# Kernel tuning notes

Measured on AMD Instinct MI355X. Metric: run time of the kernel, lower is better.

Reference implementation:

```python
import jax, jax.numpy as jnp
import numpy as np

B, T, C, L, NH = 2, 512, 512, 3, 8
SD, AD, MT = 65, 17, 4096  # state_dim+1, act_dim+1, max_timestep
H4 = 4 * C
S = 3 * T
D = C // NH


def setup_inputs() -> dict:
    key = jax.random.key(0)
    keys = iter(jax.random.split(key, 64))

    def p(*shape):
        return jax.random.normal(next(keys), shape, dtype=jnp.float32) * 0.02

    inp = {
        "timesteps": jax.random.randint(next(keys), (B, T), 0, MT),
        "states": jax.random.randint(next(keys), (B, T), 0, SD),
        "actions": jax.random.randint(next(keys), (B, T), 0, AD),
        "returns_to_go": jax.random.normal(next(keys), (B, T, 1), dtype=jnp.float32),
        # embeddings / input projections
        "Wt": p(MT, C), "Ws": p(SD, C), "Wa": p(AD, C),
        "Wr_w": p(C, 1), "Wr_b": p(C),
        "ln_e_g": jnp.ones((C,), jnp.float32), "ln_e_b": jnp.zeros((C,), jnp.float32),
        # per-block params, stacked on leading L axis (torch Linear: y = x @ W.T + b)
        "Wq": p(L, C, C), "bq": p(L, C), "Wk": p(L, C, C), "bk": p(L, C),
        "Wv": p(L, C, C), "bv": p(L, C), "Wo": p(L, C, C), "bo": p(L, C),
        "W1": p(L, H4, C), "b1": p(L, H4), "W2": p(L, C, H4), "b2": p(L, C),
        "ln1_g": jnp.ones((L, C), jnp.float32), "ln1_b": jnp.zeros((L, C), jnp.float32),
        "ln2_g": jnp.ones((L, C), jnp.float32), "ln2_b": jnp.zeros((L, C), jnp.float32),
        # prediction heads
        "pr_w": p(1, C), "pr_b": p(1),
        "ps_w": p(SD, C), "ps_b": p(SD),
        "pa_w": p(AD, C), "pa_b": p(AD),
    }
    return inp


def _ln(x, g, b):
    m = jnp.mean(x, axis=-1, keepdims=True)
    v = jnp.mean((x - m) ** 2, axis=-1, keepdims=True)
    return (x - m) / jnp.sqrt(v + 1e-5) * g + b


def _block_causal_mask(s):
    # blocks of 3 (attend within rtg/state/action triple) OR lower-triangular
    i = jnp.arange(s)
    return ((i[:, None] // 3) == (i[None, :] // 3)) | (i[:, None] >= i[None, :])


def reference(timesteps, states, actions, returns_to_go,
              Wt, Ws, Wa, Wr_w, Wr_b, ln_e_g, ln_e_b,
              Wq, bq, Wk, bk, Wv, bv, Wo, bo,
              W1, b1, W2, b2, ln1_g, ln1_b, ln2_g, ln2_b,
              pr_w, pr_b, ps_w, ps_b, pa_w, pa_b):
    te = Wt[timesteps]                                  # [B,T,C]
    se = Ws[states] + te
    ae = Wa[actions] + te
    re = returns_to_go @ Wr_w.T + Wr_b + te
    # interleave (rtg, state, action) per timestep -> [B, 3T, C]
    h = jnp.stack((re, se, ae), axis=2).reshape(B, S, C)
    h = _ln(h, ln_e_g, ln_e_b)

    mask = _block_causal_mask(S)                        # [S,S] bool
    scale = 1.0 / np.sqrt(D)
    all_w, all_m = [], []
    for l in range(L):
        q = (h @ Wq[l].T + bq[l]).reshape(B, S, NH, D).transpose(0, 2, 1, 3)
        k = (h @ Wk[l].T + bk[l]).reshape(B, S, NH, D).transpose(0, 2, 1, 3)
        v = (h @ Wv[l].T + bv[l]).reshape(B, S, NH, D).transpose(0, 2, 1, 3)
        scores = jnp.einsum('bnsd,bntd->bnst', q, k) * scale
        scores = jnp.where(mask, scores, -jnp.inf)
        w = jax.nn.softmax(scores, axis=-1)             # [B,NH,S,S]
        att = jnp.einsum('bnst,bntd->bnsd', w, v).transpose(0, 2, 1, 3).reshape(B, S, C)
        h = h + (att @ Wo[l].T + bo[l])
        h = _ln(h, ln1_g[l], ln1_b[l])
        m = jax.nn.gelu(h @ W1[l].T + b1[l], approximate=False)  # [B,S,4C]
        h = h + (m @ W2[l].T + b2[l])
        h = _ln(h, ln2_g[l], ln2_b[l])
        all_w.append(w)
        all_m.append(m)

    # faithful to original: reshape splits seq into 3 contiguous chunks of T
    hr = h.reshape(B, 3, T, C)
    rtg_preds = hr[:, 2] @ pr_w.T + pr_b                # [B,T,1]
    state_preds = hr[:, 2] @ ps_w.T + ps_b              # [B,T,SD]
    action_preds = hr[:, 1] @ pa_w.T + pa_b             # [B,T,AD] (discrete -> no tanh)
    return (state_preds, action_preds, rtg_preds, jnp.stack(all_w), jnp.stack(all_m))
```

## Files before the change

kernel.cpp:

```cpp
#include <hip/hip_runtime.h>
#include <hip/hip_bf16.h>
#include <math.h>

#define B_ 2
#define T_ 512
#define C_ 512
#define L_ 3
#define NH_ 8
#define SD_ 65
#define AD_ 17
#define H4_ 2048
#define S_ 1536
#define D_ 64

typedef __hip_bfloat16 bf16;
typedef __bf16 bf16x8 __attribute__((ext_vector_type(8)));
typedef __bf16 bf16x4 __attribute__((ext_vector_type(4)));
typedef float f32x4 __attribute__((ext_vector_type(4)));

#define OFF_STATE  0
#define OFF_ACTION 66560
#define OFF_RTG    83968
#define OFF_W      84992
#define OFF_M      113331200ULL
#define OUT_TOTAL  132205568ULL

#define WS_HF     0ULL
#define WS_HB     6291456ULL
#define WS_QK     9437184ULL
#define WS_VT     15728640ULL
#define WS_WB     18874368ULL
#define WS_BIAS   25165824ULL
#define WS_MB     25171968ULL
#define WOFF_O    (3 * C_ * C_)
#define WOFF_1    (4 * C_ * C_)
#define WOFF_2    (4 * C_ * C_ + H4_ * C_)
#define WCONV_N   (4 * C_ * C_ + 2 * H4_ * C_)

__device__ __forceinline__ __bf16 tobf(float v) {
    union { __hip_bfloat16 h; __bf16 b; } u;
    u.h = __float2bfloat16(v);
    return u.b;
}

__device__ __forceinline__ void gload_lds16(const bf16* g, bf16* l) {
    __builtin_amdgcn_global_load_lds(
        (const __attribute__((address_space(1))) void*)g,
        (__attribute__((address_space(3))) void*)l,
        16, 0, 0);
}

#define MFMA_(a, b, c) __builtin_amdgcn_mfma_f32_16x16x32_bf16(a, b, c, 0, 0, 0)

__device__ __forceinline__ void block_reduce2(float& s1, float& s2, float* lds) {
    for (int off = 32; off >= 1; off >>= 1) {
        s1 += __shfl_xor(s1, off, 64);
        s2 += __shfl_xor(s2, off, 64);
    }
    int wave = threadIdx.x >> 6;
    if ((threadIdx.x & 63) == 0) { lds[wave] = s1; lds[wave + 4] = s2; }
    __syncthreads();
    s1 = lds[0] + lds[1] + lds[2] + lds[3];
    s2 = lds[4] + lds[5] + lds[6] + lds[7];
}

__global__ __launch_bounds__(256) void convw_kernel(
    const float* __restrict__ Wq, const float* __restrict__ Wk,
    const float* __restrict__ Wv, const float* __restrict__ Wo,
    const float* __restrict__ W1, const float* __restrict__ W2,
    const float* __restrict__ bq, const float* __restrict__ bk, const float* __restrict__ bv,
    bf16* __restrict__ dst, float* __restrict__ pbias)
{
    int i = (blockIdx.x * 256 + threadIdx.x) * 4;
    const float* src; int off;
    if      (i <     C_ * C_)            { src = Wq; off = i; }
    else if (i < 2 * C_ * C_)            { src = Wk; off = i -     C_ * C_; }
    else if (i < 3 * C_ * C_)            { src = Wv; off = i - 2 * C_ * C_; }
    else if (i < 4 * C_ * C_)            { src = Wo; off = i - 3 * C_ * C_; }
    else if (i < 4 * C_ * C_ + H4_ * C_) { src = W1; off = i - 4 * C_ * C_; }
    else                                 { src = W2; off = i - 4 * C_ * C_ - H4_ * C_; }
    f32x4 v = *(const f32x4*)(src + off);
    bf16x4 o;
#pragma unroll
    for (int j = 0; j < 4; j++) o[j] = tobf(v[j]);
    *(bf16x4*)(dst + i) = o;
    if (blockIdx.x == 0) {
        for (int j = threadIdx.x; j < 3 * C_; j += 256)
            pbias[j] = (j < C_) ? bq[j] : (j < 2 * C_) ? bk[j - C_] : bv[j - 2 * C_];
    }
}

__global__ __launch_bounds__(256) void embed_kernel(
    const int* __restrict__ timesteps, const int* __restrict__ states,
    const int* __restrict__ actions, const float* __restrict__ rtg,
    const float* __restrict__ Wt, const float* __restrict__ Ws, const float* __restrict__ Wa,
    const float* __restrict__ Wr_w, const float* __restrict__ Wr_b,
    const float* __restrict__ g, const float* __restrict__ bta,
    float* __restrict__ h, bf16* __restrict__ hb)
{
    int bid = blockIdx.x;
    int b = bid / S_, s = bid % S_;
    int t = s / 3, kind = s % 3;
    int tid = threadIdx.x;
    int bt = b * T_ + t;
    float vals[2];
    float s1 = 0.f, s2 = 0.f;
    int ts = timesteps[bt];
    for (int i = 0; i < 2; i++) {
        int c = tid + i * 256;
        float te = Wt[(size_t)ts * C_ + c];
        float v;
        if (kind == 0)
            v = rtg[bt] * Wr_w[c] + Wr_b[c] + te;
        else if (kind == 1)
            v = Ws[(size_t)states[bt] * C_ + c] + te;
        else
            v = Wa[(size_t)actions[bt] * C_ + c] + te;
        vals[i] = v; s1 += v; s2 += v * v;
    }
    __shared__ float lds[8];
    block_reduce2(s1, s2, lds);
    float mean = s1 / C_;
    float rstd = rsqrtf(s2 / C_ - mean * mean + 1e-5f);
    size_t rowoff = (size_t)bid * C_;
    for (int i = 0; i < 2; i++) {
        int c = tid + i * 256;
        float o = (vals[i] - mean) * rstd * g[c] + bta[c];
        h[rowoff + c] = o;
        hb[rowoff + c] = __float2bfloat16(o);
    }
}

__global__ __launch_bounds__(256) void ln_kernel(
    float* __restrict__ h, const float* __restrict__ g, const float* __restrict__ bta,
    bf16* __restrict__ hb)
{
    int bid = blockIdx.x;
    int tid = threadIdx.x;
    size_t rowoff = (size_t)bid * C_;
    float vals[2]; float s1 = 0.f, s2 = 0.f;
    for (int i = 0; i < 2; i++) {
        float v = h[rowoff + tid + i * 256];
        vals[i] = v; s1 += v; s2 += v * v;
    }
    __shared__ float lds[8];
    block_reduce2(s1, s2, lds);
    float mean = s1 / C_;
    float rstd = rsqrtf(s2 / C_ - mean * mean + 1e-5f);
    for (int i = 0; i < 2; i++) {
        int c = tid + i * 256;
        float o = (vals[i] - mean) * rstd * g[c] + bta[c];
        h[rowoff + c] = o;
        hb[rowoff + c] = __float2bfloat16(o);
    }
}

__global__ __launch_bounds__(256) void gemm_st_kernel(
    const bf16* __restrict__ A, const bf16* __restrict__ W,
    const float* __restrict__ bias, int M, int N, int K, int epi,
    bf16* __restrict__ out_bf, bf16* __restrict__ vT,
    float* __restrict__ out_f32, bf16* __restrict__ out_bfs)
{
    __shared__ bf16 lA[2][128 * 64];
    __shared__ bf16 lB[2][64 * 64];
    int tid = threadIdx.x;
    int wave = tid >> 6, lane = tid & 63;
    int quad = lane >> 4, l16 = lane & 15;
    int m0 = blockIdx.y * 128;
    int n0 = blockIdx.x * 64;
    int lrow = lane >> 3;
    int lcol = (lane & 7) * 8;
    const bf16* Ag = A + (size_t)m0 * K;
    const bf16* Wg = W + (size_t)n0 * K;
    f32x4 acc[4][2] = {};
    int NT = K / 64;

#pragma unroll
    for (int jj = 0; jj < 4; jj++) {
        int q = wave * 4 + jj;
        gload_lds16(Ag + (size_t)(q * 8 + lrow) * K + lcol, &lA[0][q * 512]);
    }
#pragma unroll
    for (int jj = 0; jj < 2; jj++) {
        int q = wave * 2 + jj;
        gload_lds16(Wg + (size_t)(q * 8 + lrow) * K + lcol, &lB[0][q * 512]);
    }
    __syncthreads();

    int rw = wave >> 1, cw = wave & 1;
    for (int t = 0; t < NT; t++) {
        int cur = t & 1, nxt = cur ^ 1;
        if (t + 1 < NT) {
            int k0 = (t + 1) * 64;
#pragma unroll
            for (int jj = 0; jj < 4; jj++) {
                int q = wave * 4 + jj;
                gload_lds16(Ag + (size_t)(q * 8 + lrow) * K + k0 + lcol, &lA[nxt][q * 512]);
            }
#pragma unroll
            for (int jj = 0; jj < 2; jj++) {
                int q = wave * 2 + jj;
                gload_lds16(Wg + (size_t)(q * 8 + lrow) * K + k0 + lcol, &lB[nxt][q * 512]);
            }
        }
#pragma unroll
        for (int ks = 0; ks < 2; ks++) {
            bf16x8 bfr0 = *(const bf16x8*)(&lB[cur][(cw * 32 + l16) * 64 + ks * 32 + quad * 8]);
            bf16x8 bfr1 = *(const bf16x8*)(&lB[cur][(cw * 32 + 16 + l16) * 64 + ks * 32 + quad * 8]);
#pragma unroll
            for (int mf = 0; mf < 4; mf++) {
                bf16x8 afr = *(const bf16x8*)(&lA[cur][(rw * 64 + mf * 16 + l16) * 64 + ks * 32 + quad * 8]);
                acc[mf][0] = MFMA_(afr, bfr0, acc[mf][0]);
                acc[mf][1] = MFMA_(afr, bfr1, acc[mf][1]);
            }
        }
        __syncthreads();
    }

#pragma unroll
    for (int mf = 0; mf < 4; mf++)
#pragma unroll
    for (int nf = 0; nf < 2; nf++) {
        int col = n0 + cw * 32 + nf * 16 + l16;
        float bia = bias ? bias[col] : 0.f;
#pragma unroll
        for (int r = 0; r < 4; r++) {
            int row = m0 + rw * 64 + mf * 16 + quad * 4 + r;
            float v = acc[mf][nf][r] + bia;
            if (epi == 0) {
                if (col < 1024) {
                    out_bf[(size_t)row * 1024 + col] = __float2bfloat16(v);
                } else {
                    int c = col - 1024;
                    int bb = row / S_, ss = row % S_;
                    vT[(((size_t)bb * NH_ + (c >> 6)) * D_ + (c & 63)) * S_ + ss] = __float2bfloat16(v);
                }
            } else if (epi == 2) {
                size_t idx = (size_t)row * N + col;
                out_f32[idx] = v + out_f32[idx];
            } else {
                size_t idx = (size_t)row * N + col;
                float gl = 0.5f * v * (1.f + erff(v * 0.70710678f));
                out_f32[idx] = gl;
                out_bfs[idx] = __float2bfloat16(gl);
            }
        }
    }
}

__global__ __launch_bounds__(256) void attn_kernel(
    const bf16* __restrict__ qk, const bf16* __restrict__ vT,
    float* __restrict__ w_out, bf16* __restrict__ att)
{
    int strip = blockIdx.x;
    int bh = blockIdx.y;
    int b = bh / NH_, h = bh % NH_;
    int s0 = strip * 16;
    int tid = threadIdx.x;
    int wave = tid >> 6, lane = tid & 63, quad = lane >> 4, l16 = lane & 15;
    int ja = 3 * ((s0 + 15) / 3) + 2;
    int jtiles = ja / 16 + 1;
    int jlen32 = ((jtiles * 16) + 31) & ~31;
    __shared__ bf16 sc[16][1576];

    const bf16* qrow = qk + ((size_t)(b * S_ + s0 + l16)) * 1024 + h * D_ + quad * 8;
    bf16x8 a0 = *(const bf16x8*)(qrow);
    bf16x8 a1 = *(const bf16x8*)(qrow + 32);
    for (int jt = wave; jt < jtiles; jt += 4) {
        const bf16* krow = qk + ((size_t)(b * S_ + jt * 16 + l16)) * 1024 + 512 + h * D_ + quad * 8;
        bf16x8 b0 = *(const bf16x8*)(krow);
        bf16x8 b1 = *(const bf16x8*)(krow + 32);
        f32x4 acc = {0.f, 0.f, 0.f, 0.f};
        acc = MFMA_(a0, b0, acc);
        acc = MFMA_(a1, b1, acc);
        for (int r = 0; r < 4; r++)
            sc[quad * 4 + r][jt * 16 + l16] = __float2bfloat16(acc[r] * 0.125f);
    }
    __syncthreads();

    {
        int r = tid >> 4, c0 = (tid & 15) * 4;
        int i = s0 + r;
        int lim = 3 * (i / 3) + 2;
        float m = -3.0e38f;
        for (int c = c0; c <= lim; c += 64) {
#pragma unroll
            for (int j = 0; j < 4; j++) {
                int cc = c + j;
                if (cc <= lim) m = fmaxf(m, __bfloat162float(sc[r][cc]));
            }
        }
        for (int off = 8; off >= 1; off >>= 1) m = fmaxf(m, __shfl_xor(m, off, 16));
        float sum = 0.f;
        for (int c = c0; c <= lim; c += 64) {
#pragma unroll
            for (int j = 0; j < 4; j++) {
                int cc = c + j;
                if (cc <= lim) sum += __expf(__bfloat162float(sc[r][cc]) - m);
            }
        }
        for (int off = 8; off >= 1; off >>= 1) sum += __shfl_xor(sum, off, 16);
        float inv = 1.f / sum;
        float* wrow = w_out + ((size_t)bh * S_ + i) * S_;
        for (int c = c0; c < S_; c += 64) {
            f32x4 o;
#pragma unroll
            for (int j = 0; j < 4; j++) {
                int cc = c + j;
                o[j] = (cc <= lim) ? __expf(__bfloat162float(sc[r][cc]) - m) * inv : 0.f;
            }
            if (c < jlen32) {
                bf16x4 p;
#pragma unroll
                for (int j = 0; j < 4; j++) p[j] = tobf(o[j]);
                *(bf16x4*)(&sc[r][c]) = p;
            }
            *(f32x4*)(wrow + c) = o;
        }
    }
    __syncthreads();

    const bf16* vbase = vT + ((size_t)bh * D_ + wave * 16 + l16) * S_ + quad * 8;
    const bf16* arow = &sc[l16][quad * 8];
    f32x4 acc = {0.f, 0.f, 0.f, 0.f};
    for (int k0 = 0; k0 < jlen32; k0 += 32) {
        bf16x8 a = *(const bf16x8*)(arow + k0);
        bf16x8 bv = *(const bf16x8*)(vbase + k0);
        acc = MFMA_(a, bv, acc);
    }
    for (int r = 0; r < 4; r++) {
        int s = s0 + quad * 4 + r;
        int d = wave * 16 + l16;
        att[((size_t)(b * S_ + s)) * C_ + h * D_ + d] = __float2bfloat16(acc[r]);
    }
}

__global__ __launch_bounds__(256) void heads_kernel(
    const float* __restrict__ h,
    const float* __restrict__ pr_w, const float* __restrict__ pr_b,
    const float* __restrict__ ps_w, const float* __restrict__ ps_b,
    const float* __restrict__ pa_w, const float* __restrict__ pa_b,
    float* __restrict__ out)
{
    int bid = blockIdx.x;
    int b = bid / T_, t = bid % T_;
    __shared__ float hs[C_], ha[C_];
    int tid = threadIdx.x;
    for (int i = tid; i < C_; i += 256) {
        hs[i] = h[((size_t)(b * S_ + 2 * T_ + t)) * C_ + i];
        ha[i] = h[((size_t)(b * S_ + T_ + t)) * C_ + i];
    }
    __syncthreads();
    if (tid < SD_) {
        float acc = ps_b[tid];
        for (int kk = 0; kk < C_; kk++) acc += ps_w[tid * C_ + kk] * hs[kk];
        out[OFF_STATE + ((size_t)(b * T_ + t)) * SD_ + tid] = acc;
    } else if (tid < SD_ + AD_) {
        int n = tid - SD_;
        float acc = pa_b[n];
        for (int kk = 0; kk < C_; kk++) acc += pa_w[n * C_ + kk] * ha[kk];
        out[OFF_ACTION + ((size_t)(b * T_ + t)) * AD_ + n] = acc;
    } else if (tid == SD_ + AD_) {
        float acc = pr_b[0];
        for (int kk = 0; kk < C_; kk++) acc += pr_w[kk] * hs[kk];
        out[OFF_RTG + (size_t)(b * T_ + t)] = acc;
    }
}

extern "C" void kernel_launch(void* const* d_in, const int* in_sizes, int n_in,
                              void* d_out, int out_size, void* d_ws, size_t ws_size,
                              hipStream_t stream) {
    const int* timesteps = (const int*)d_in[0];
    const int* states    = (const int*)d_in[1];
    const int* actions   = (const int*)d_in[2];
    const float* rtg    = (const float*)d_in[3];
    const float* Wt     = (const float*)d_in[4];
    const float* Ws     = (const float*)d_in[5];
    const float* Wa     = (const float*)d_in[6];
    const float* Wr_w   = (const float*)d_in[7];
    const float* Wr_b   = (const float*)d_in[8];
    const float* ln_e_g = (const float*)d_in[9];
    const float* ln_e_b = (const float*)d_in[10];
    const float* Wq     = (const float*)d_in[11];
    const float* bq     = (const float*)d_in[12];
    const float* Wk     = (const float*)d_in[13];
    const float* bk     = (const float*)d_in[14];
    const float* Wv     = (const float*)d_in[15];
    const float* bv     = (const float*)d_in[16];
    const float* Wo     = (const float*)d_in[17];
    const float* bo     = (const float*)d_in[18];
    const float* W1     = (const float*)d_in[19];
    const float* b1     = (const float*)d_in[20];
    const float* W2     = (const float*)d_in[21];
    const float* b2     = (const float*)d_in[22];
    const float* ln1_g  = (const float*)d_in[23];
    const float* ln1_b  = (const float*)d_in[24];
    const float* ln2_g  = (const float*)d_in[25];
    const float* ln2_b  = (const float*)d_in[26];
    const float* pr_w   = (const float*)d_in[27];
    const float* pr_b   = (const float*)d_in[28];
    const float* ps_w   = (const float*)d_in[29];
    const float* ps_b   = (const float*)d_in[30];
    const float* pa_w   = (const float*)d_in[31];
    const float* pa_b   = (const float*)d_in[32];

    float* out = (float*)d_out;
    char* ws = (char*)d_ws;
    float* h_f   = (float*)(ws + WS_HF);
    bf16* h_bf   = (bf16*)(ws + WS_HB);
    bf16* qk_bf  = (bf16*)(ws + WS_QK);
    bf16* vT     = (bf16*)(ws + WS_VT);
    bf16* Wbf    = (bf16*)(ws + WS_WB);
    float* pbias = (float*)(ws + WS_BIAS);
    bf16* m_bf   = (bf16*)(ws + WS_MB);
    bf16* att_bf = m_bf;

    const int M = B_ * S_;

    embed_kernel<<<B_ * S_, 256, 0, stream>>>(timesteps, states, actions, rtg,
                                              Wt, Ws, Wa, Wr_w, Wr_b, ln_e_g, ln_e_b,
                                              h_f, h_bf);

    for (int l = 0; l < L_; l++) {
        const float* Wq_l = Wq + (size_t)l * C_ * C_;
        const float* Wk_l = Wk + (size_t)l * C_ * C_;
        const float* Wv_l = Wv + (size_t)l * C_ * C_;
        const float* Wo_l = Wo + (size_t)l * C_ * C_;
        const float* W1_l = W1 + (size_t)l * H4_ * C_;
        const float* W2_l = W2 + (size_t)l * C_ * H4_;
        float* w_l = out + OFF_W + (size_t)l * B_ * NH_ * (size_t)S_ * S_;
        float* m_l = out + OFF_M + (size_t)l * B_ * S_ * H4_;

        convw_kernel<<<WCONV_N / 4 / 256, 256, 0, stream>>>(
            Wq_l, Wk_l, Wv_l, Wo_l, W1_l, W2_l,
            bq + l * C_, bk + l * C_, bv + l * C_, Wbf, pbias);

        gemm_st_kernel<<<dim3(24, 24), 256, 0, stream>>>(
            h_bf, Wbf, pbias, M, 1536, C_, 0, qk_bf, vT, nullptr, nullptr);

        attn_kernel<<<dim3(S_ / 16, B_ * NH_), 256, 0, stream>>>(qk_bf, vT, w_l, att_bf);

        gemm_st_kernel<<<dim3(8, 24), 256, 0, stream>>>(
            att_bf, Wbf + WOFF_O, bo + l * C_, M, C_, C_, 2, nullptr, nullptr, h_f, nullptr);
        ln_kernel<<<B_ * S_, 256, 0, stream>>>(h_f, ln1_g + l * C_, ln1_b + l * C_, h_bf);

        gemm_st_kernel<<<dim3(32, 24), 256, 0, stream>>>(
            h_bf, Wbf + WOFF_1, b1 + l * H4_, M, H4_, C_, 3, nullptr, nullptr, m_l, m_bf);
        gemm_st_kernel<<<dim3(8, 24), 256, 0, stream>>>(
            m_bf, Wbf + WOFF_2, b2 + l * C_, M, C_, H4_, 2, nullptr, nullptr, h_f, nullptr);
        ln_kernel<<<B_ * S_, 256, 0, stream>>>(h_f, ln2_g + l * C_, ln2_b + l * C_, h_bf);
    }

    heads_kernel<<<B_ * T_, 256, 0, stream>>>(h_f, pr_w, pr_b, ps_w, ps_b, pa_w, pa_b, out);
}
```

Baseline: 1.149 ms.

## Template GEMM M-tile, stage V transpose via LDS, reverse attention strip order

The GEMM kernel is templated on its M-tile height, and the two N=512 projections (output projection and MLP down-projection) switch to 64-row tiles. This doubles their grid to use more of the GPU's compute units, at the cost of less A/B reuse per block. The QKV epilogue now writes the transposed V through an LDS staging buffer, giving coalesced 16-byte stores instead of scattered per-element writes. The attention grid is reversed so the longest causal strips launch first, to reduce tail imbalance.

```diff
diff --git a/kernel.cpp b/kernel.cpp
--- a/kernel.cpp
+++ b/kernel.cpp
@@ -155,29 +155,31 @@
     }
 }
 
+template<int BMF>
 __global__ __launch_bounds__(256) void gemm_st_kernel(
     const bf16* __restrict__ A, const bf16* __restrict__ W,
     const float* __restrict__ bias, int M, int N, int K, int epi,
     bf16* __restrict__ out_bf, bf16* __restrict__ vT,
     float* __restrict__ out_f32, bf16* __restrict__ out_bfs)
 {
-    __shared__ bf16 lA[2][128 * 64];
+    constexpr int BM = 32 * BMF;
+    __shared__ bf16 lA[2][BM * 64];
     __shared__ bf16 lB[2][64 * 64];
     int tid = threadIdx.x;
     int wave = tid >> 6, lane = tid & 63;
     int quad = lane >> 4, l16 = lane & 15;
-    int m0 = blockIdx.y * 128;
+    int m0 = blockIdx.y * BM;
     int n0 = blockIdx.x * 64;
     int lrow = lane >> 3;
     int lcol = (lane & 7) * 8;
     const bf16* Ag = A + (size_t)m0 * K;
     const bf16* Wg = W + (size_t)n0 * K;
-    f32x4 acc[4][2] = {};
+    f32x4 acc[BMF][2] = {};
     int NT = K / 64;
 
 #pragma unroll
-    for (int jj = 0; jj < 4; jj++) {
-        int q = wave * 4 + jj;
+    for (int jj = 0; jj < BMF; jj++) {
+        int q = wave * BMF + jj;
         gload_lds16(Ag + (size_t)(q * 8 + lrow) * K + lcol, &lA[0][q * 512]);
     }
 #pragma unroll
@@ -193,8 +195,8 @@
         if (t + 1 < NT) {
             int k0 = (t + 1) * 64;
 #pragma unroll
-            for (int jj = 0; jj < 4; jj++) {
-                int q = wave * 4 + jj;
+            for (int jj = 0; jj < BMF; jj++) {
+                int q = wave * BMF + jj;
                 gload_lds16(Ag + (size_t)(q * 8 + lrow) * K + k0 + lcol, &lA[nxt][q * 512]);
             }
 #pragma unroll
@@ -208,8 +210,8 @@
             bf16x8 bfr0 = *(const bf16x8*)(&lB[cur][(cw * 32 + l16) * 64 + ks * 32 + quad * 8]);
             bf16x8 bfr1 = *(const bf16x8*)(&lB[cur][(cw * 32 + 16 + l16) * 64 + ks * 32 + quad * 8]);
 #pragma unroll
-            for (int mf = 0; mf < 4; mf++) {
-                bf16x8 afr = *(const bf16x8*)(&lA[cur][(rw * 64 + mf * 16 + l16) * 64 + ks * 32 + quad * 8]);
+            for (int mf = 0; mf < BMF; mf++) {
+                bf16x8 afr = *(const bf16x8*)(&lA[cur][(rw * (BM / 2) + mf * 16 + l16) * 64 + ks * 32 + quad * 8]);
                 acc[mf][0] = MFMA_(afr, bfr0, acc[mf][0]);
                 acc[mf][1] = MFMA_(afr, bfr1, acc[mf][1]);
             }
@@ -217,29 +219,62 @@
         __syncthreads();
     }
 
-#pragma unroll
-    for (int mf = 0; mf < 4; mf++)
+    if (epi == 0) {
+        if constexpr (BMF == 4) {
+            if (n0 >= 1024) {
+                bf16* sT = &lA[0][0];
+#pragma unroll
+                for (int mf = 0; mf < 4; mf++)
+#pragma unroll
+                for (int nf = 0; nf < 2; nf++) {
+                    int dl = cw * 32 + nf * 16 + l16;
+                    float bia = bias[n0 + dl];
+#pragma unroll
+                    for (int r = 0; r < 4; r++) {
+                        int sl = rw * 64 + mf * 16 + quad * 4 + r;
+                        sT[dl * 136 + sl] = __float2bfloat16(acc[mf][nf][r] + bia);
+                    }
+                }
+                __syncthreads();
+                int b = m0 / S_, s0 = m0 % S_;
+                int h = (n0 - 1024) >> 6;
+                int d = tid >> 2, qs = (tid & 3) * 32;
+                bf16* dst = vT + (((size_t)b * NH_ + h) * D_ + d) * S_ + s0 + qs;
+#pragma unroll
+                for (int j = 0; j < 4; j++)
+                    *(bf16x8*)(dst + j * 8) = *(const bf16x8*)(&sT[d * 136 + qs + j * 8]);
+                return;
+            }
+        }
+#pragma unroll
+        for (int mf = 0; mf < BMF; mf++)
+#pragma unroll
+        for (int nf = 0; nf < 2; nf++) {
+            int col = n0 + cw * 32 + nf * 16 + l16;
+            float bia = bias[col];
+#pragma unroll
+            for (int r = 0; r < 4; r++) {
+                int row = m0 + rw * (BM / 2) + mf * 16 + quad * 4 + r;
+                out_bf[(size_t)row * 1024 + col] = __float2bfloat16(acc[mf][nf][r] + bia);
+            }
+        }
+        return;
+    }
+
+#pragma unroll
+    for (int mf = 0; mf < BMF; mf++)
 #pragma unroll
     for (int nf = 0; nf < 2; nf++) {
         int col = n0 + cw * 32 + nf * 16 + l16;
         float bia = bias ? bias[col] : 0.f;
 #pragma unroll
         for (int r = 0; r < 4; r++) {
-            int row = m0 + rw * 64 + mf * 16 + quad * 4 + r;
+            int row = m0 + rw * (BM / 2) + mf * 16 + quad * 4 + r;
             float v = acc[mf][nf][r] + bia;
-            if (epi == 0) {
-                if (col < 1024) {
-                    out_bf[(size_t)row * 1024 + col] = __float2bfloat16(v);
-                } else {
-                    int c = col - 1024;
-                    int bb = row / S_, ss = row % S_;
-                    vT[(((size_t)bb * NH_ + (c >> 6)) * D_ + (c & 63)) * S_ + ss] = __float2bfloat16(v);
-                }
-            } else if (epi == 2) {
-                size_t idx = (size_t)row * N + col;
+            size_t idx = (size_t)row * N + col;
+            if (epi == 2) {
                 out_f32[idx] = v + out_f32[idx];
             } else {
-                size_t idx = (size_t)row * N + col;
                 float gl = 0.5f * v * (1.f + erff(v * 0.70710678f));
                 out_f32[idx] = gl;
                 out_bfs[idx] = __float2bfloat16(gl);
@@ -252,7 +287,7 @@
     const bf16* __restrict__ qk, const bf16* __restrict__ vT,
     float* __restrict__ w_out, bf16* __restrict__ att)
 {
-    int strip = blockIdx.x;
+    int strip = (S_ / 16 - 1) - blockIdx.x;
     int bh = blockIdx.y;
     int b = bh / NH_, h = bh % NH_;
     int s0 = strip * 16;
@@ -435,18 +470,18 @@
             Wq_l, Wk_l, Wv_l, Wo_l, W1_l, W2_l,
             bq + l * C_, bk + l * C_, bv + l * C_, Wbf, pbias);
 
-        gemm_st_kernel<<<dim3(24, 24), 256, 0, stream>>>(
+        gemm_st_kernel<4><<<dim3(24, 24), 256, 0, stream>>>(
             h_bf, Wbf, pbias, M, 1536, C_, 0, qk_bf, vT, nullptr, nullptr);
 
         attn_kernel<<<dim3(S_ / 16, B_ * NH_), 256, 0, stream>>>(qk_bf, vT, w_l, att_bf);
 
-        gemm_st_kernel<<<dim3(8, 24), 256, 0, stream>>>(
+        gemm_st_kernel<2><<<dim3(8, 48), 256, 0, stream>>>(
             att_bf, Wbf + WOFF_O, bo + l * C_, M, C_, C_, 2, nullptr, nullptr, h_f, nullptr);
         ln_kernel<<<B_ * S_, 256, 0, stream>>>(h_f, ln1_g + l * C_, ln1_b + l * C_, h_bf);
 
-        gemm_st_kernel<<<dim3(32, 24), 256, 0, stream>>>(
+        gemm_st_kernel<4><<<dim3(32, 24), 256, 0, stream>>>(
             h_bf, Wbf + WOFF_1, b1 + l * H4_, M, H4_, C_, 3, nullptr, nullptr, m_l, m_bf);
-        gemm_st_kernel<<<dim3(8, 24), 256, 0, stream>>>(
+        gemm_st_kernel<2><<<dim3(8, 48), 256, 0, stream>>>(
             m_bf, Wbf + WOFF_2, b2 + l * C_, M, C_, H4_, 2, nullptr, nullptr, h_f, nullptr);
         ln_kernel<<<B_ * S_, 256, 0, stream>>>(h_f, ln2_g + l * C_, ln2_b + l * C_, h_bf);
     }
```

After: 1.085 ms. 1.06x faster.
